# Kernel tuning notes

Measured on AMD Instinct MI355X. Metric: run time of the kernel, lower is better.

Reference implementation:

```python
import jax, jax.numpy as jnp
import numpy as np

EMB = 512
HEADS = 8

def setup_inputs() -> dict:
    key = jax.random.key(0)
    ks = jax.random.split(key, 9)
    s = 1.0 / np.sqrt(EMB)
    return {
        'x':  jax.random.normal(ks[0], (4, 2048, EMB), dtype=jnp.float32),
        'Wq': jax.random.uniform(ks[1], (EMB, EMB), jnp.float32, -s, s),
        'bq': jax.random.uniform(ks[2], (EMB,), jnp.float32, -s, s),
        'Wk': jax.random.uniform(ks[3], (EMB, EMB), jnp.float32, -s, s),
        'bk': jax.random.uniform(ks[4], (EMB,), jnp.float32, -s, s),
        'Wv': jax.random.uniform(ks[5], (EMB, EMB), jnp.float32, -s, s),
        'bv': jax.random.uniform(ks[6], (EMB,), jnp.float32, -s, s),
        'Wo': jax.random.uniform(ks[7], (EMB, EMB), jnp.float32, -s, s),
        'bo': jax.random.uniform(ks[8], (EMB,), jnp.float32, -s, s),
    }

def reference(x, Wq, bq, Wk, bk, Wv, bv, Wo, bo):
    b, n, e = x.shape
    h = HEADS
    d = e // h
    def split_heads(t):
        return t.reshape(b, n, h, d).transpose(0, 2, 1, 3)  # b h n d
    q = split_heads(x @ Wq.T + bq)
    k = split_heads(x @ Wk.T + bk)
    v = split_heads(x @ Wv.T + bv)
    energy = jnp.einsum('bhqd,bhkd->bhqk', q, k)
    scaling = jnp.sqrt(jnp.float32(e))  # NOTE: sqrt(emb_size), not sqrt(head_dim), per source
    att = jax.nn.softmax(energy / scaling, axis=-1)
    out = jnp.einsum('bhal,bhlv->bhav', att, v)  # b h n d
    out = out.transpose(0, 2, 1, 3).reshape(b, n, e)
    return out @ Wo.T + bo
```

## Files before the change

### kernel.cpp

```cpp
#include <hip/hip_runtime.h>

typedef float f32x4 __attribute__((ext_vector_type(4)));
typedef float f32x16 __attribute__((ext_vector_type(16)));
typedef short bf16x8 __attribute__((ext_vector_type(8)));
typedef unsigned int uint;
typedef unsigned short ushort_t;

#define EMB    512
#define NSEQ   2048
#define NBATCH 4
#define NHEAD  8
#define MROWS  (NBATCH * NSEQ)
#define CEXP   0.06375872f

__device__ __forceinline__ uint f2bf(float x) {
    uint u = __builtin_bit_cast(uint, x);
    return (u + 0x7fffu + ((u >> 16) & 1u)) >> 16;
}

__device__ __forceinline__ void glds16(const void* g, void* l) {
    __builtin_amdgcn_global_load_lds(
        (const __attribute__((address_space(1))) uint*)g,
        (__attribute__((address_space(3))) uint*)l, 16, 0, 0);
}

__global__ __launch_bounds__(256)
void prep(const float* __restrict__ x,
          const float* __restrict__ Wq, const float* __restrict__ Wk,
          const float* __restrict__ Wv, const float* __restrict__ Wo,
          const float* __restrict__ bq, const float* __restrict__ bk,
          const float* __restrict__ bv,
          ushort_t* __restrict__ xb, ushort_t* __restrict__ Wqkvb,
          float* __restrict__ bqkv, ushort_t* __restrict__ Wob) {
    int t = blockIdx.x * 256 + threadIdx.x;
    {
        float4 v = ((const float4*)x)[t];
        uint2 p;
        p.x = f2bf(v.x) | (f2bf(v.y) << 16);
        p.y = f2bf(v.z) | (f2bf(v.w) << 16);
        ((uint2*)xb)[t] = p;
    }
    if (t < 65536) {
        float4 a = ((const float4*)Wq)[t];
        float4 b = ((const float4*)Wk)[t];
        float4 c = ((const float4*)Wv)[t];
        float4 d = ((const float4*)Wo)[t];
        uint2 p;
        p.x = f2bf(a.x) | (f2bf(a.y) << 16); p.y = f2bf(a.z) | (f2bf(a.w) << 16);
        ((uint2*)Wqkvb)[t] = p;
        p.x = f2bf(b.x) | (f2bf(b.y) << 16); p.y = f2bf(b.z) | (f2bf(b.w) << 16);
        ((uint2*)Wqkvb)[t + 65536] = p;
        p.x = f2bf(c.x) | (f2bf(c.y) << 16); p.y = f2bf(c.z) | (f2bf(c.w) << 16);
        ((uint2*)Wqkvb)[t + 131072] = p;
        p.x = f2bf(d.x) | (f2bf(d.y) << 16); p.y = f2bf(d.z) | (f2bf(d.w) << 16);
        ((uint2*)Wob)[t] = p;
    }
    if (t < 512) {
        bqkv[t] = bq[t]; bqkv[512 + t] = bk[t]; bqkv[1024 + t] = bv[t];
    }
}

template<int MODE>
__global__ __launch_bounds__(256)
void gemm128(const ushort_t* __restrict__ A, const ushort_t* __restrict__ BT,
             const float* __restrict__ bias, ushort_t* __restrict__ oQK,
             ushort_t* __restrict__ oVT, float* __restrict__ oC) {
    __shared__ ushort_t As[2][128][32];
    __shared__ ushort_t Bs[2][128][32];
    __shared__ float ep[32][132];
    const int tid = threadIdx.x, wave = tid >> 6, lane = tid & 63;
    const int m0 = blockIdx.x * 128, n0 = blockIdx.y * 128;
    const int wr = (wave & 1) * 64, wc = (wave >> 1) * 64;

    f32x4 acc[4][4];
#pragma unroll
    for (int i = 0; i < 4; ++i)
#pragma unroll
        for (int j = 0; j < 4; ++j) acc[i][j] = (f32x4){0.f, 0.f, 0.f, 0.f};

    const int grow = wave * 16 + (lane >> 2);
    const int gcol = (lane & 3) * 8;
    const ushort_t* Ag = A  + (size_t)(m0 + grow) * 512 + gcol;
    const ushort_t* Bg = BT + (size_t)(n0 + grow) * 512 + gcol;
    const int fr = lane & 15, fc = (lane >> 4) * 8;

    for (int kt = 0; kt < 8; ++kt) {
        __syncthreads();
#pragma unroll
        for (int t = 0; t < 2; ++t) {
            glds16(Ag + kt * 64 + t * 32,            &As[t][wave * 16][0]);
            glds16(Ag + kt * 64 + t * 32 + 64 * 512, &As[t][64 + wave * 16][0]);
            glds16(Bg + kt * 64 + t * 32,            &Bs[t][wave * 16][0]);
            glds16(Bg + kt * 64 + t * 32 + 64 * 512, &Bs[t][64 + wave * 16][0]);
        }
        __syncthreads();
#pragma unroll
        for (int t = 0; t < 2; ++t) {
            bf16x8 af[4], bf[4];
#pragma unroll
            for (int i = 0; i < 4; ++i) af[i] = *(const bf16x8*)&As[t][wr + i * 16 + fr][fc];
#pragma unroll
            for (int j = 0; j < 4; ++j) bf[j] = *(const bf16x8*)&Bs[t][wc + j * 16 + fr][fc];
#pragma unroll
            for (int i = 0; i < 4; ++i)
#pragma unroll
                for (int j = 0; j < 4; ++j)
                    acc[i][j] = __builtin_amdgcn_mfma_f32_16x16x32_bf16(af[i], bf[j], acc[i][j], 0, 0, 0);
        }
    }

    const int col_l = lane & 15, row_l = (lane >> 4) * 4;

    if (MODE == 0 && n0 >= 1024) {
#pragma unroll
        for (int j = 0; j < 4; ++j) {
            const int col = n0 + wc + j * 16 + col_l;
            const float bv = bias[col];
#pragma unroll
            for (int i = 0; i < 4; ++i) {
                const int row = m0 + wr + i * 16 + row_l;
                f32x4 v = acc[i][j];
                v += (f32x4){bv, bv, bv, bv};
                const int e = col - 1024;
                const int b = row >> 11, tok = row & 2047;
                uint2 p;
                p.x = f2bf(v[0]) | (f2bf(v[1]) << 16);
                p.y = f2bf(v[2]) | (f2bf(v[3]) << 16);
                *(uint2*)&oVT[((size_t)(b * 512 + e)) * 2048 + tok] = p;
            }
        }
        return;
    }

    const float scale = (MODE == 0 && n0 < 512) ? CEXP : 1.0f;
    float bv[4];
#pragma unroll
    for (int j = 0; j < 4; ++j) bv[j] = bias[n0 + wc + j * 16 + col_l];

    const int erow = tid >> 3, eseg = (tid & 7) * 16;
#pragma unroll
    for (int c = 0; c < 4; ++c) {
        __syncthreads();
        if (wr == (c >> 1) * 64) {
#pragma unroll
            for (int ii = 0; ii < 2; ++ii) {
                const int i = (c & 1) * 2 + ii;
#pragma unroll
                for (int j = 0; j < 4; ++j) {
                    f32x4 v = acc[i][j];
#pragma unroll
                    for (int r = 0; r < 4; ++r)
                        ep[ii * 16 + row_l + r][wc + j * 16 + col_l] = (v[r] + bv[j]) * scale;
                }
            }
        }
        __syncthreads();
        const int grow2 = m0 + c * 32 + erow;
        if (MODE == 0) {
            uint4 o0, o1;
#pragma unroll
            for (int k = 0; k < 4; ++k) {
                uint lo = f2bf(ep[erow][eseg + k * 2])     | (f2bf(ep[erow][eseg + k * 2 + 1]) << 16);
                uint hi = f2bf(ep[erow][eseg + 8 + k * 2]) | (f2bf(ep[erow][eseg + 9 + k * 2]) << 16);
                ((uint*)&o0)[k] = lo; ((uint*)&o1)[k] = hi;
            }
            *(uint4*)&oQK[(size_t)grow2 * 1024 + n0 + eseg]     = o0;
            *(uint4*)&oQK[(size_t)grow2 * 1024 + n0 + eseg + 8] = o1;
        } else {
#pragma unroll
            for (int k = 0; k < 4; ++k) {
                f32x4 v = *(const f32x4*)&ep[erow][eseg + k * 4];
                *(f32x4*)&oC[(size_t)grow2 * 512 + n0 + eseg + k * 4] = v;
            }
        }
    }
}

template<int NSLICE>
__global__ __launch_bounds__(256, 2)
void attn_mfma(const ushort_t* __restrict__ QK, const ushort_t* __restrict__ VT,
               ushort_t* __restrict__ Op, float* __restrict__ Lp,
               ushort_t* __restrict__ AO) {
    __shared__ ushort_t Ks[64][72];
    __shared__ ushort_t Vs[64][72];

    const int tid = threadIdx.x, w = tid >> 6, lane = tid & 63;
    const int qt = blockIdx.x, bh = blockIdx.y, b = bh >> 3, h = bh & 7;
    const int slice = (NSLICE > 1) ? blockIdx.z : 0;
    const int l31 = lane & 31, lhi = lane >> 5;

    const int tok0 = qt * 256 + w * 64 + l31;
    bf16x8 qf[2][4];
#pragma unroll
    for (int g = 0; g < 2; ++g)
#pragma unroll
        for (int ks = 0; ks < 4; ++ks)
            qf[g][ks] = *(const bf16x8*)&QK[(size_t)(b * NSEQ + tok0 + g * 32) * 1024
                                            + h * 64 + ks * 16 + lhi * 8];

    f32x16 accO[2][2];
    f32x16 accL[2];
#pragma unroll
    for (int g = 0; g < 2; ++g) {
#pragma unroll
        for (int i = 0; i < 16; ++i) { accO[g][0][i] = 0.f; accO[g][1][i] = 0.f; accL[g][i] = 0.f; }
    }
    union { uint u[4]; bf16x8 v; } ONE;
    ONE.u[0] = 0x3f803f80u; ONE.u[1] = 0x3f803f80u;
    ONE.u[2] = 0x3f803f80u; ONE.u[3] = 0x3f803f80u;

    const int sr = tid & 63, sc = (tid >> 6) * 16;
    const ushort_t* Kg = QK + (size_t)(b * NSEQ) * 1024 + 512 + h * 64;
    const ushort_t* Vg = VT + ((size_t)(b * 512 + h * 64)) * 2048;

    const int kt0 = slice * (32 / NSLICE), kt1 = kt0 + 32 / NSLICE;
    for (int kt = kt0; kt < kt1; ++kt) {
        const int k0 = kt * 64;
        uint4 kv0 = *(const uint4*)&Kg[(size_t)(k0 + sr) * 1024 + sc];
        uint4 kv1 = *(const uint4*)&Kg[(size_t)(k0 + sr) * 1024 + sc + 8];
        uint4 vv0 = *(const uint4*)&Vg[(size_t)sr * 2048 + k0 + sc];
        uint4 vv1 = *(const uint4*)&Vg[(size_t)sr * 2048 + k0 + sc + 8];
        __syncthreads();
        *(uint4*)&Ks[sr][sc] = kv0;  *(uint4*)&Ks[sr][sc + 8] = kv1;
        *(uint4*)&Vs[sr][sc] = vv0;  *(uint4*)&Vs[sr][sc + 8] = vv1;
        __syncthreads();

#pragma unroll
        for (int ms = 0; ms < 2; ++ms) {
            bf16x8 ka[4];
#pragma unroll
            for (int ks = 0; ks < 4; ++ks)
                ka[ks] = *(const bf16x8*)&Ks[ms * 32 + l31][ks * 16 + lhi * 8];

            f32x16 st[2];
#pragma unroll
            for (int g = 0; g < 2; ++g)
#pragma unroll
                for (int i = 0; i < 16; ++i) st[g][i] = 0.f;
#pragma unroll
            for (int ks = 0; ks < 4; ++ks) {
                st[0] = __builtin_amdgcn_mfma_f32_32x32x16_bf16(ka[ks], qf[0][ks], st[0], 0, 0, 0);
                st[1] = __builtin_amdgcn_mfma_f32_32x32x16_bf16(ka[ks], qf[1][ks], st[1], 0, 0, 0);
            }

            uint dd[2][8], ee[2][8];
#pragma unroll
            for (int g = 0; g < 2; ++g)
#pragma unroll
                for (int i = 0; i < 8; ++i) {
                    uint ua = __builtin_bit_cast(uint, __builtin_amdgcn_exp2f(st[g][2 * i]));
                    uint ub = __builtin_bit_cast(uint, __builtin_amdgcn_exp2f(st[g][2 * i + 1]));
                    dd[g][i] = (ua >> 16) | (ub & 0xffff0000u);
                }
#pragma unroll
            for (int g = 0; g < 2; ++g)
#pragma unroll
                for (int i = 0; i < 8; ++i)
                    ee[g][i] = (uint)__shfl_xor((int)dd[g][i], 32);

#pragma unroll
            for (int s = 0; s < 2; ++s) {
                const int step = ms * 2 + s;
                bf16x8 va0 = *(const bf16x8*)&Vs[l31][step * 16 + lhi * 8];
                bf16x8 va1 = *(const bf16x8*)&Vs[32 + l31][step * 16 + lhi * 8];
#pragma unroll
                for (int g = 0; g < 2; ++g) {
                    union { uint u[4]; bf16x8 v; } B;
                    B.u[0] = lhi ? ee[g][4 * s + 2] : dd[g][4 * s + 0];
                    B.u[1] = lhi ? ee[g][4 * s + 3] : dd[g][4 * s + 1];
                    B.u[2] = lhi ? dd[g][4 * s + 2] : ee[g][4 * s + 0];
                    B.u[3] = lhi ? dd[g][4 * s + 3] : ee[g][4 * s + 1];
                    accO[g][0] = __builtin_amdgcn_mfma_f32_32x32x16_bf16(va0, B.v, accO[g][0], 0, 0, 0);
                    accO[g][1] = __builtin_amdgcn_mfma_f32_32x32x16_bf16(va1, B.v, accO[g][1], 0, 0, 0);
                    accL[g]    = __builtin_amdgcn_mfma_f32_32x32x16_bf16(ONE.v, B.v, accL[g], 0, 0, 0);
                }
            }
        }
    }

    if (NSLICE == 1) {
#pragma unroll
        for (int g = 0; g < 2; ++g) {
            const float inv = 1.0f / accL[g][0];
#pragma unroll
            for (int hf = 0; hf < 2; ++hf)
#pragma unroll
                for (int r = 0; r < 16; ++r) {
                    const int d = (r & 3) + 8 * (r >> 2) + 4 * lhi + 32 * hf;
                    AO[((size_t)(b * NSEQ + tok0 + g * 32)) * 512 + h * 64 + d] =
                        (ushort_t)f2bf(accO[g][hf][r] * inv);
                }
        }
    } else {
        if (lane < 32) {
#pragma unroll
            for (int g = 0; g < 2; ++g)
                Lp[(size_t)slice * 65536 + bh * 2048 + tok0 + g * 32] = accL[g][0];
        }
        ushort_t* Os = Op + (size_t)slice * 4194304;
#pragma unroll
        for (int g = 0; g < 2; ++g)
#pragma unroll
            for (int hf = 0; hf < 2; ++hf)
#pragma unroll
                for (int r = 0; r < 16; ++r) {
                    const int d = (r & 3) + 8 * (r >> 2) + 4 * lhi + 32 * hf;
                    Os[((size_t)(bh * 64 + d)) * 2048 + tok0 + g * 32] =
                        (ushort_t)f2bf(accO[g][hf][r]);
                }
    }
}

__global__ __launch_bounds__(256)
void combine2Tb(const ushort_t* __restrict__ Op, const float* __restrict__ Lp,
                ushort_t* __restrict__ AO) {
    __shared__ float T[64][68];
    const int tid = threadIdx.x;
    const int tc = blockIdx.x, bh = blockIdx.y;
    const int b = bh >> 3, h = bh & 7;
    const int tok0 = tc * 64;

    const int d = tid >> 2, ts = (tid & 3) * 16;
    float acc[16];
#pragma unroll
    for (int i = 0; i < 16; ++i) acc[i] = 0.f;
#pragma unroll
    for (int s = 0; s < 2; ++s) {
        const ushort_t* P = Op + (size_t)s * 4194304
                               + ((size_t)(bh * 64 + d)) * 2048 + tok0 + ts;
#pragma unroll
        for (int k2 = 0; k2 < 2; ++k2) {
            uint4 u = *(const uint4*)(P + 8 * k2);
#pragma unroll
            for (int j = 0; j < 4; ++j) {
                uint uw = ((const uint*)&u)[j];
                acc[k2 * 8 + 2 * j]     += __builtin_bit_cast(float, uw << 16);
                acc[k2 * 8 + 2 * j + 1] += __builtin_bit_cast(float, uw & 0xffff0000u);
            }
        }
    }
#pragma unroll
    for (int k = 0; k < 4; ++k)
        *(f32x4*)&T[d][ts + 4 * k] = *(const f32x4*)&acc[4 * k];
    __syncthreads();

    const int tk = tid >> 2, ds = (tid & 3) * 16;
    const int tok = tok0 + tk;
    const float inv = 1.0f / (Lp[bh * 2048 + tok] + Lp[65536 + bh * 2048 + tok]);
    uint o[8];
#pragma unroll
    for (int k = 0; k < 8; ++k) {
        float a = T[ds + 2 * k][tk] * inv;
        float c = T[ds + 2 * k + 1][tk] * inv;
        o[k] = f2bf(a) | (f2bf(c) << 16);
    }
    ushort_t* dst = AO + ((size_t)(b * NSEQ + tok)) * 512 + h * 64 + ds;
    *(uint4*)dst       = *(const uint4*)&o[0];
    *(uint4*)(dst + 8) = *(const uint4*)&o[4];
}

extern "C" void kernel_launch(void* const* d_in, const int* in_sizes, int n_in,
                              void* d_out, int out_size, void* d_ws, size_t ws_size,
                              hipStream_t stream) {
    const float* x  = (const float*)d_in[0];
    const float* Wq = (const float*)d_in[1];
    const float* bq = (const float*)d_in[2];
    const float* Wk = (const float*)d_in[3];
    const float* bk = (const float*)d_in[4];
    const float* Wv = (const float*)d_in[5];
    const float* bv = (const float*)d_in[6];
    const float* Wo = (const float*)d_in[7];
    const float* bo = (const float*)d_in[8];

    char* ws = (char*)d_ws;
    ushort_t* xb    = (ushort_t*)(ws);
    ushort_t* Wqkvb = (ushort_t*)(ws + 8388608);
    ushort_t* Wob   = (ushort_t*)(ws + 9961472);
    float*    bqkv  = (float*)   (ws + 10485760);
    ushort_t* QKb   = (ushort_t*)(ws + 10491904);
    ushort_t* VTg   = (ushort_t*)(ws + 27269120);
    ushort_t* AOb   = (ushort_t*)(ws + 35657728);
    ushort_t* Opart = (ushort_t*)(ws + 44046336);
    float*    Lpart = (float*)   (ws);
    const bool split = ws_size >= 78125056;

    prep<<<4096, 256, 0, stream>>>(x, Wq, Wk, Wv, Wo, bq, bk, bv,
                                   xb, Wqkvb, bqkv, Wob);
    gemm128<0><<<dim3(64, 12), 256, 0, stream>>>(xb, Wqkvb, bqkv, QKb, VTg, nullptr);
    if (split) {
        attn_mfma<2><<<dim3(8, 32, 2), 256, 0, stream>>>(QKb, VTg, Opart, Lpart, nullptr);
        combine2Tb<<<dim3(32, 32), 256, 0, stream>>>(Opart, Lpart, AOb);
    } else {
        attn_mfma<1><<<dim3(8, 32, 1), 256, 0, stream>>>(QKb, VTg, nullptr, nullptr, AOb);
    }
    gemm128<1><<<dim3(64, 4), 256, 0, stream>>>(AOb, Wob, bo, nullptr, nullptr, (float*)d_out);
}
```

Measured before the change: 179.5 us.

## Split attention KV into four slices and retile output projection GEMM

Attention now splits the key/value range into four slices instead of two, with a combine kernel that sums four partial outputs and normalizers. Occupancy is raised via launch bounds of 4 blocks per CU. The output projection gets its own 128x64-tile kernel, doubling its block count to fill more CUs. These changes trade more partial-output traffic, extra combine work and possible register pressure for better parallelism on the 256-CU device.

```diff
diff --git a/kernel.cpp b/kernel.cpp
--- a/kernel.cpp
+++ b/kernel.cpp
@@ -60,11 +60,10 @@
     }
 }
 
-template<int MODE>
 __global__ __launch_bounds__(256)
-void gemm128(const ushort_t* __restrict__ A, const ushort_t* __restrict__ BT,
-             const float* __restrict__ bias, ushort_t* __restrict__ oQK,
-             ushort_t* __restrict__ oVT, float* __restrict__ oC) {
+void gemm_qkv(const ushort_t* __restrict__ A, const ushort_t* __restrict__ BT,
+              const float* __restrict__ bias, ushort_t* __restrict__ oQK,
+              ushort_t* __restrict__ oVT) {
     __shared__ ushort_t As[2][128][32];
     __shared__ ushort_t Bs[2][128][32];
     __shared__ float ep[32][132];
@@ -111,7 +110,7 @@
 
     const int col_l = lane & 15, row_l = (lane >> 4) * 4;
 
-    if (MODE == 0 && n0 >= 1024) {
+    if (n0 >= 1024) {
 #pragma unroll
         for (int j = 0; j < 4; ++j) {
             const int col = n0 + wc + j * 16 + col_l;
@@ -132,7 +131,7 @@
         return;
     }
 
-    const float scale = (MODE == 0 && n0 < 512) ? CEXP : 1.0f;
+    const float scale = (n0 < 512) ? CEXP : 1.0f;
     float bv[4];
 #pragma unroll
     for (int j = 0; j < 4; ++j) bv[j] = bias[n0 + wc + j * 16 + col_l];
@@ -156,28 +155,93 @@
         }
         __syncthreads();
         const int grow2 = m0 + c * 32 + erow;
-        if (MODE == 0) {
-            uint4 o0, o1;
-#pragma unroll
-            for (int k = 0; k < 4; ++k) {
-                uint lo = f2bf(ep[erow][eseg + k * 2])     | (f2bf(ep[erow][eseg + k * 2 + 1]) << 16);
-                uint hi = f2bf(ep[erow][eseg + 8 + k * 2]) | (f2bf(ep[erow][eseg + 9 + k * 2]) << 16);
-                ((uint*)&o0)[k] = lo; ((uint*)&o1)[k] = hi;
-            }
-            *(uint4*)&oQK[(size_t)grow2 * 1024 + n0 + eseg]     = o0;
-            *(uint4*)&oQK[(size_t)grow2 * 1024 + n0 + eseg + 8] = o1;
-        } else {
-#pragma unroll
-            for (int k = 0; k < 4; ++k) {
-                f32x4 v = *(const f32x4*)&ep[erow][eseg + k * 4];
-                *(f32x4*)&oC[(size_t)grow2 * 512 + n0 + eseg + k * 4] = v;
-            }
-        }
+        uint4 o0, o1;
+#pragma unroll
+        for (int k = 0; k < 4; ++k) {
+            uint lo = f2bf(ep[erow][eseg + k * 2])     | (f2bf(ep[erow][eseg + k * 2 + 1]) << 16);
+            uint hi = f2bf(ep[erow][eseg + 8 + k * 2]) | (f2bf(ep[erow][eseg + 9 + k * 2]) << 16);
+            ((uint*)&o0)[k] = lo; ((uint*)&o1)[k] = hi;
+        }
+        *(uint4*)&oQK[(size_t)grow2 * 1024 + n0 + eseg]     = o0;
+        *(uint4*)&oQK[(size_t)grow2 * 1024 + n0 + eseg + 8] = o1;
+    }
+}
+
+__global__ __launch_bounds__(256)
+void gemm_out(const ushort_t* __restrict__ A, const ushort_t* __restrict__ BT,
+              const float* __restrict__ bias, float* __restrict__ oC) {
+    __shared__ ushort_t As[2][128][32];
+    __shared__ ushort_t Bs[2][64][32];
+    __shared__ float ep[32][68];
+    const int tid = threadIdx.x, wave = tid >> 6, lane = tid & 63;
+    const int m0 = blockIdx.x * 128, n0 = blockIdx.y * 64;
+    const int wr = wave * 32;
+
+    f32x4 acc[2][4];
+#pragma unroll
+    for (int i = 0; i < 2; ++i)
+#pragma unroll
+        for (int j = 0; j < 4; ++j) acc[i][j] = (f32x4){0.f, 0.f, 0.f, 0.f};
+
+    const int grow = wave * 16 + (lane >> 2);
+    const int gcol = (lane & 3) * 8;
+    const ushort_t* Ag = A  + (size_t)(m0 + grow) * 512 + gcol;
+    const ushort_t* Bg = BT + (size_t)(n0 + grow) * 512 + gcol;
+    const int fr = lane & 15, fc = (lane >> 4) * 8;
+
+    for (int kt = 0; kt < 8; ++kt) {
+        __syncthreads();
+#pragma unroll
+        for (int t = 0; t < 2; ++t) {
+            glds16(Ag + kt * 64 + t * 32,            &As[t][wave * 16][0]);
+            glds16(Ag + kt * 64 + t * 32 + 64 * 512, &As[t][64 + wave * 16][0]);
+            glds16(Bg + kt * 64 + t * 32,            &Bs[t][wave * 16][0]);
+        }
+        __syncthreads();
+#pragma unroll
+        for (int t = 0; t < 2; ++t) {
+            bf16x8 af[2], bf[4];
+#pragma unroll
+            for (int i = 0; i < 2; ++i) af[i] = *(const bf16x8*)&As[t][wr + i * 16 + fr][fc];
+#pragma unroll
+            for (int j = 0; j < 4; ++j) bf[j] = *(const bf16x8*)&Bs[t][j * 16 + fr][fc];
+#pragma unroll
+            for (int i = 0; i < 2; ++i)
+#pragma unroll
+                for (int j = 0; j < 4; ++j)
+                    acc[i][j] = __builtin_amdgcn_mfma_f32_16x16x32_bf16(af[i], bf[j], acc[i][j], 0, 0, 0);
+        }
+    }
+
+    const int col_l = lane & 15, row_l = (lane >> 4) * 4;
+    float bv[4];
+#pragma unroll
+    for (int j = 0; j < 4; ++j) bv[j] = bias[n0 + j * 16 + col_l];
+
+    const int erow = tid >> 3, eseg = (tid & 7) * 8;
+#pragma unroll
+    for (int c = 0; c < 4; ++c) {
+        __syncthreads();
+        if (wave == c) {
+#pragma unroll
+            for (int i = 0; i < 2; ++i)
+#pragma unroll
+                for (int j = 0; j < 4; ++j) {
+                    f32x4 v = acc[i][j];
+#pragma unroll
+                    for (int r = 0; r < 4; ++r)
+                        ep[i * 16 + row_l + r][j * 16 + col_l] = v[r] + bv[j];
+                }
+        }
+        __syncthreads();
+        const int grow2 = m0 + c * 32 + erow;
+        *(f32x4*)&oC[(size_t)grow2 * 512 + n0 + eseg]     = *(const f32x4*)&ep[erow][eseg];
+        *(f32x4*)&oC[(size_t)grow2 * 512 + n0 + eseg + 4] = *(const f32x4*)&ep[erow][eseg + 4];
     }
 }
 
 template<int NSLICE>
-__global__ __launch_bounds__(256, 2)
+__global__ __launch_bounds__(256, 4)
 void attn_mfma(const ushort_t* __restrict__ QK, const ushort_t* __restrict__ VT,
                ushort_t* __restrict__ Op, float* __restrict__ Lp,
                ushort_t* __restrict__ AO) {
@@ -312,8 +376,8 @@
 }
 
 __global__ __launch_bounds__(256)
-void combine2Tb(const ushort_t* __restrict__ Op, const float* __restrict__ Lp,
-                ushort_t* __restrict__ AO) {
+void combine4T(const ushort_t* __restrict__ Op, const float* __restrict__ Lp,
+               ushort_t* __restrict__ AO) {
     __shared__ float T[64][68];
     const int tid = threadIdx.x;
     const int tc = blockIdx.x, bh = blockIdx.y;
@@ -325,7 +389,7 @@
 #pragma unroll
     for (int i = 0; i < 16; ++i) acc[i] = 0.f;
 #pragma unroll
-    for (int s = 0; s < 2; ++s) {
+    for (int s = 0; s < 4; ++s) {
         const ushort_t* P = Op + (size_t)s * 4194304
                                + ((size_t)(bh * 64 + d)) * 2048 + tok0 + ts;
 #pragma unroll
@@ -346,7 +410,9 @@
 
     const int tk = tid >> 2, ds = (tid & 3) * 16;
     const int tok = tok0 + tk;
-    const float inv = 1.0f / (Lp[bh * 2048 + tok] + Lp[65536 + bh * 2048 + tok]);
+    const float l = Lp[bh * 2048 + tok]           + Lp[65536 + bh * 2048 + tok]
+                  + Lp[131072 + bh * 2048 + tok]  + Lp[196608 + bh * 2048 + tok];
+    const float inv = 1.0f / l;
     uint o[8];
 #pragma unroll
     for (int k = 0; k < 8; ++k) {
@@ -386,12 +452,12 @@
 
     prep<<<4096, 256, 0, stream>>>(x, Wq, Wk, Wv, Wo, bq, bk, bv,
                                    xb, Wqkvb, bqkv, Wob);
-    gemm128<0><<<dim3(64, 12), 256, 0, stream>>>(xb, Wqkvb, bqkv, QKb, VTg, nullptr);
+    gemm_qkv<<<dim3(64, 12), 256, 0, stream>>>(xb, Wqkvb, bqkv, QKb, VTg);
     if (split) {
-        attn_mfma<2><<<dim3(8, 32, 2), 256, 0, stream>>>(QKb, VTg, Opart, Lpart, nullptr);
-        combine2Tb<<<dim3(32, 32), 256, 0, stream>>>(Opart, Lpart, AOb);
+        attn_mfma<4><<<dim3(8, 32, 4), 256, 0, stream>>>(QKb, VTg, Opart, Lpart, nullptr);
+        combine4T<<<dim3(32, 32), 256, 0, stream>>>(Opart, Lpart, AOb);
     } else {
         attn_mfma<1><<<dim3(8, 32, 1), 256, 0, stream>>>(QKb, VTg, nullptr, nullptr, AOb);
     }
-    gemm128<1><<<dim3(64, 4), 256, 0, stream>>>(AOb, Wob, bo, nullptr, nullptr, (float*)d_out);
-}
+    gemm_out<<<dim3(64, 8), 256, 0, stream>>>(AOb, Wob, bo, (float*)d_out);
+}
```

Result: slower. 559.7 us (+211.8%).
